# Optimization experiments

Hardware: AMD Instinct MI355X
Metric: run time of the kernel (lower is better)

The kernel has to match this reference:

```python
import jax, jax.numpy as jnp
import numpy as np

# SMPL kinematic tree (24 joints); edge (parent -> child) for each child with parent >= 0
SMPL_PARENTS = np.array([-1, 0, 0, 0, 1, 2, 3, 4, 5, 6, 7, 8, 9, 9, 9, 12, 13, 14, 16, 17, 18, 19, 20, 21])
J = 24            # SMPL_NR_JOINTS
IN_DIM = 3        # input_dim
HID = 24          # hidden_dim
HEADS = 3
OUT = HID // HEADS  # 8 per-head channels; concat -> 24
N, L = 64, 2048
NEG_SLOPE = 0.2   # PyG GATConv default LeakyReLU slope


def _batched_edges(num_frames):
    """Tree edges replicated per (batch, time) frame with node-index offsets."""
    mask = SMPL_PARENTS >= 0
    parent = SMPL_PARENTS[mask]            # source nodes
    child = np.arange(J)[mask]             # destination nodes
    base = np.stack([parent, child])       # (2, 23)
    off = np.arange(num_frames) * J        # (num_frames,)
    edges = base[:, None, :] + off[None, :, None]   # (2, num_frames, 23)
    return edges.reshape(2, -1).astype(np.int32)


def setup_inputs() -> dict:
    key = jax.random.key(0)
    ks = jax.random.split(key, 7)
    s_pre = 1.0 / np.sqrt(IN_DIM)
    s_gat = 1.0 / np.sqrt(HID)
    return {
        "src": jax.random.normal(ks[0], (N, L, J * IN_DIM), dtype=jnp.float32),
        "W_pre": jax.random.normal(ks[1], (IN_DIM, HID), dtype=jnp.float32) * s_pre,
        "b_pre": jax.random.normal(ks[2], (HID,), dtype=jnp.float32) * s_pre,
        "W_gat": jax.random.normal(ks[3], (HID, HEADS * OUT), dtype=jnp.float32) * s_gat,
        "att_src": jax.random.normal(ks[4], (HEADS, OUT), dtype=jnp.float32) * s_gat,
        "att_dst": jax.random.normal(ks[5], (HEADS, OUT), dtype=jnp.float32) * s_gat,
        "b_gat": jax.random.normal(ks[6], (HEADS * OUT,), dtype=jnp.float32) * s_gat,
    }


def reference(src, W_pre, b_pre, W_gat, att_src, att_dst, b_gat):
    n, l, d = src.shape
    num_frames = n * l
    nn = num_frames * J                       # total nodes
    x = src.reshape(nn, IN_DIM)
    x = jax.nn.relu(x @ W_pre + b_pre)        # (nn, 24)

    # GATConv (shared lin for src/dst since single in_channels)
    h = (x @ W_gat).reshape(nn, HEADS, OUT)   # (nn, H, O)
    a_src = jnp.einsum('nho,ho->nh', h, att_src)  # (nn, H)
    a_dst = jnp.einsum('nho,ho->nh', h, att_dst)

    tree = jnp.asarray(_batched_edges(num_frames))          # (2, 23*frames)
    loops = jnp.arange(nn, dtype=jnp.int32)                  # PyG default add_self_loops=True
    src_i = jnp.concatenate([tree[0], loops])
    dst_i = jnp.concatenate([tree[1], loops])

    e = jax.nn.leaky_relu(a_src[src_i] + a_dst[dst_i], NEG_SLOPE)   # (E, H)
    m = jax.ops.segment_max(e, dst_i, num_segments=nn)
    ex = jnp.exp(e - m[dst_i])
    denom = jax.ops.segment_sum(ex, dst_i, num_segments=nn)
    alpha = ex / denom[dst_i]                                       # segment softmax over dst

    out = jax.ops.segment_sum(alpha[:, :, None] * h[src_i], dst_i, num_segments=nn)  # (nn, H, O)
    out = out.reshape(nn, HEADS * OUT) + b_gat
    out = jax.nn.relu(out)
    return out.reshape(n, l, J * HID)
```

## Files before the change

kernel.cpp:

```cpp
#include <hip/hip_runtime.h>


#define JNT 24
#define FPB 8
#define TPB (FPB*JNT)
#define NPB (FPB*JNT)
#define NT  16384
#define GRID 1280

__constant__ int c_par[JNT] = {-1,0,0,0,1,2,3,4,5,6,7,8,9,9,9,12,13,14,16,17,18,19,20,21};

__device__ __forceinline__ int hoff(int r) { return r*28 + ((r>>3)<<2); }

#define SH_SIZE 5468

#define BAR() do { asm volatile("s_waitcnt lgkmcnt(0)" ::: "memory"); \
                   __builtin_amdgcn_s_barrier(); } while (0)

__global__ __launch_bounds__(TPB, 4)
void gat_encoder(const float* __restrict__ src,
                 const float* __restrict__ W_pre,
                 const float* __restrict__ b_pre,
                 const float* __restrict__ W_gat,
                 const float* __restrict__ att_src,
                 const float* __restrict__ att_dst,
                 const float* __restrict__ b_gat,
                 float* __restrict__ out)
{
    __shared__ int   s_par[JNT];
    __shared__ __align__(16) float s_h[SH_SIZE];

    const int tid = threadIdx.x;
    if (tid < JNT) s_par[tid] = c_par[tid];

    int tile = blockIdx.x;

    const float* sg = src + (size_t)tile * (NPB*3) + tid*3;
    float p0 = sg[0], p1 = sg[1], p2 = sg[2];

    while (tile < NT) {
        const int nxt = tile + GRID;
        const float* ng = src + (size_t)(nxt < NT ? nxt : tile) * (NPB*3) + tid*3;
        float q0 = ng[0], q1 = ng[1], q2 = ng[2];

        float h[JNT];
        #pragma unroll
        for (int o = 0; o < JNT; ++o) h[o] = 0.f;

        #pragma unroll 2
        for (int k = 0; k < JNT; ++k) {
            const float w0 = W_pre[k], w1 = W_pre[24+k], w2 = W_pre[48+k];
            const float bb = b_pre[k];
            float x = fmaf(p0, w0, fmaf(p1, w1, fmaf(p2, w2, bb)));
            x = fmaxf(x, 0.f);
            #pragma unroll
            for (int o = 0; o < JNT; ++o)
                h[o] = fmaf(x, W_gat[k*JNT + o], h[o]);
        }

        float as[3], ad[3];
        #pragma unroll
        for (int hd = 0; hd < 3; ++hd) {
            float a = 0.f, d = 0.f;
            #pragma unroll
            for (int o = 0; o < 8; ++o) {
                a = fmaf(h[hd*8+o], att_src[hd*8+o], a);
                d = fmaf(h[hd*8+o], att_dst[hd*8+o], d);
            }
            as[hd] = a; ad[hd] = d;
        }

        float* hr = &s_h[hoff(tid)];
        #pragma unroll
        for (int q = 0; q < 6; ++q)
            ((float4*)hr)[q] = make_float4(h[q*4+0], h[q*4+1], h[q*4+2], h[q*4+3]);
        hr[24] = as[0]; hr[25] = as[1]; hr[26] = as[2];
        BAR();

        const int  f    = tid / JNT;
        const int  j    = tid - f*JNT;
        const int  par  = s_par[j];
        const bool hasp = (par >= 0);
        const float* hp = &s_h[hoff(f*JNT + (hasp ? par : j))];

        float ws[3], wpv[3];
        #pragma unroll
        for (int hd = 0; hd < 3; ++hd) {
            float es = as[hd] + ad[hd];      es = es < 0.f ? 0.2f*es : es;
            float ep = hp[24+hd] + ad[hd];   ep = ep < 0.f ? 0.2f*ep : ep;
            float m  = hasp ? fmaxf(es, ep) : es;
            float e1 = __expf(es - m);
            float e2 = hasp ? __expf(ep - m) : 0.f;
            float r  = 1.f / (e1 + e2);
            ws[hd] = e1*r; wpv[hd] = e2*r;
        }

        float r[JNT];
        #pragma unroll
        for (int q = 0; q < 6; ++q) {
            const int hd = q >> 1;
            const float4 p4 = ((const float4*)hp)[q];
            r[q*4+0] = fmaxf(fmaf(wpv[hd], p4.x, fmaf(ws[hd], h[q*4+0], b_gat[q*4+0])), 0.f);
            r[q*4+1] = fmaxf(fmaf(wpv[hd], p4.y, fmaf(ws[hd], h[q*4+1], b_gat[q*4+1])), 0.f);
            r[q*4+2] = fmaxf(fmaf(wpv[hd], p4.z, fmaf(ws[hd], h[q*4+2], b_gat[q*4+2])), 0.f);
            r[q*4+3] = fmaxf(fmaf(wpv[hd], p4.w, fmaf(ws[hd], h[q*4+3], b_gat[q*4+3])), 0.f);
        }

        BAR();
        {
            float* orow = &s_h[tid*28];
            #pragma unroll
            for (int q = 0; q < 6; ++q)
                ((float4*)orow)[q] = make_float4(r[q*4+0], r[q*4+1], r[q*4+2], r[q*4+3]);
        }
        BAR();

        {
            const int n0 = (tid*4) / JNT;
            const int c0 = (tid*4) % JNT;
            const float* rb = &s_h[n0*28 + c0];
            float4 v[6];
            #pragma unroll
            for (int k = 0; k < 6; ++k)
                v[k] = *(const float4*)(rb + k*896);
            float* og = out + (size_t)tile * (NPB*JNT) + tid*4;
            #pragma unroll
            for (int k = 0; k < 6; ++k)
                *(float4*)(og + k*768) = v[k];
        }

        BAR();
        p0 = q0; p1 = q1; p2 = q2;
        tile = nxt;
    }
}

extern "C" void kernel_launch(void* const* d_in, const int* in_sizes, int n_in,
                              void* d_out, int out_size, void* d_ws, size_t ws_size,
                              hipStream_t stream) {
    const float* src     = (const float*)d_in[0];
    const float* W_pre   = (const float*)d_in[1];
    const float* b_pre   = (const float*)d_in[2];
    const float* W_gat   = (const float*)d_in[3];
    const float* att_src = (const float*)d_in[4];
    const float* att_dst = (const float*)d_in[5];
    const float* b_gat   = (const float*)d_in[6];
    float* out = (float*)d_out;

    gat_encoder<<<dim3(GRID), dim3(TPB), 0, stream>>>(
        src, W_pre, b_pre, W_gat, att_src, att_dst, b_gat, out);
}
```

Before: 360.6 us.

## Switch to one-wave blocks of two frames and packed float2 math

The persistent grid-stride kernel with 8-frame, 192-thread blocks and register prefetch is replaced by a non-persistent launch of 65536 single-wave blocks, each handling two frames (48 active lanes of 64). The dense projections and aggregation are rewritten with two-wide float vector types so the compiler can emit packed FMA instructions. The intent is to cut per-instruction ALU cost and let the hardware scheduler hide latency across many small blocks. In exchange, a quarter of the lanes sit idle in compute, the cross-tile prefetch is lost, and launch/block scheduling overhead rises.

```diff
diff --git a/kernel.cpp b/kernel.cpp
--- a/kernel.cpp
+++ b/kernel.cpp
@@ -1,18 +1,19 @@
 #include <hip/hip_runtime.h>
 
 
+typedef float f32x2 __attribute__((ext_vector_type(2)));
+
 #define JNT 24
-#define FPB 8
-#define TPB (FPB*JNT)
-#define NPB (FPB*JNT)
-#define NT  16384
-#define GRID 1280
+#define FPW 2
+#define TPB 64
+#define ACT (FPW*JNT)
+#define OUTD (ACT*JNT)
 
 __constant__ int c_par[JNT] = {-1,0,0,0,1,2,3,4,5,6,7,8,9,9,9,12,13,14,16,17,18,19,20,21};
 
 __device__ __forceinline__ int hoff(int r) { return r*28 + ((r>>3)<<2); }
 
-#define SH_SIZE 5468
+#define SH_SIZE 1364
 
 #define BAR() do { asm volatile("s_waitcnt lgkmcnt(0)" ::: "memory"); \
                    __builtin_amdgcn_s_barrier(); } while (0)
@@ -31,21 +32,20 @@
     __shared__ __align__(16) float s_h[SH_SIZE];
 
     const int tid = threadIdx.x;
+    const int blk = blockIdx.x;
+    const bool act = tid < ACT;
+
     if (tid < JNT) s_par[tid] = c_par[tid];
 
-    int tile = blockIdx.x;
+    f32x2 h2[12];
+    float as[3], ad[3];
 
-    const float* sg = src + (size_t)tile * (NPB*3) + tid*3;
-    float p0 = sg[0], p1 = sg[1], p2 = sg[2];
+    if (act) {
+        const float* sg = src + (size_t)blk * (ACT*3) + tid*3;
+        const float p0 = sg[0], p1 = sg[1], p2 = sg[2];
 
-    while (tile < NT) {
-        const int nxt = tile + GRID;
-        const float* ng = src + (size_t)(nxt < NT ? nxt : tile) * (NPB*3) + tid*3;
-        float q0 = ng[0], q1 = ng[1], q2 = ng[2];
-
-        float h[JNT];
         #pragma unroll
-        for (int o = 0; o < JNT; ++o) h[o] = 0.f;
+        for (int o = 0; o < 12; ++o) h2[o] = (f32x2){0.f, 0.f};
 
         #pragma unroll 2
         for (int k = 0; k < JNT; ++k) {
@@ -53,31 +53,38 @@
             const float bb = b_pre[k];
             float x = fmaf(p0, w0, fmaf(p1, w1, fmaf(p2, w2, bb)));
             x = fmaxf(x, 0.f);
+            const f32x2 xx = (f32x2){x, x};
+            const f32x2* wr = (const f32x2*)(W_gat + k*JNT);
             #pragma unroll
-            for (int o = 0; o < JNT; ++o)
-                h[o] = fmaf(x, W_gat[k*JNT + o], h[o]);
+            for (int o = 0; o < 12; ++o)
+                h2[o] = xx * wr[o] + h2[o];
         }
 
-        float as[3], ad[3];
         #pragma unroll
         for (int hd = 0; hd < 3; ++hd) {
-            float a = 0.f, d = 0.f;
+            f32x2 a2 = (f32x2){0.f, 0.f}, d2 = (f32x2){0.f, 0.f};
+            const f32x2* asr = (const f32x2*)(att_src + hd*8);
+            const f32x2* adr = (const f32x2*)(att_dst + hd*8);
             #pragma unroll
-            for (int o = 0; o < 8; ++o) {
-                a = fmaf(h[hd*8+o], att_src[hd*8+o], a);
-                d = fmaf(h[hd*8+o], att_dst[hd*8+o], d);
+            for (int o = 0; o < 4; ++o) {
+                a2 = h2[hd*4+o] * asr[o] + a2;
+                d2 = h2[hd*4+o] * adr[o] + d2;
             }
-            as[hd] = a; ad[hd] = d;
+            as[hd] = a2.x + a2.y;
+            ad[hd] = d2.x + d2.y;
         }
 
         float* hr = &s_h[hoff(tid)];
         #pragma unroll
         for (int q = 0; q < 6; ++q)
-            ((float4*)hr)[q] = make_float4(h[q*4+0], h[q*4+1], h[q*4+2], h[q*4+3]);
+            ((float4*)hr)[q] = make_float4(h2[2*q].x, h2[2*q].y, h2[2*q+1].x, h2[2*q+1].y);
         hr[24] = as[0]; hr[25] = as[1]; hr[26] = as[2];
-        BAR();
+    }
+    BAR();
 
-        const int  f    = tid / JNT;
+    f32x2 r2[12];
+    if (act) {
+        const int  f    = tid >= JNT;
         const int  j    = tid - f*JNT;
         const int  par  = s_par[j];
         const bool hasp = (par >= 0);
@@ -95,43 +102,49 @@
             ws[hd] = e1*r; wpv[hd] = e2*r;
         }
 
-        float r[JNT];
+        const f32x2* bg = (const f32x2*)b_gat;
         #pragma unroll
         for (int q = 0; q < 6; ++q) {
             const int hd = q >> 1;
             const float4 p4 = ((const float4*)hp)[q];
-            r[q*4+0] = fmaxf(fmaf(wpv[hd], p4.x, fmaf(ws[hd], h[q*4+0], b_gat[q*4+0])), 0.f);
-            r[q*4+1] = fmaxf(fmaf(wpv[hd], p4.y, fmaf(ws[hd], h[q*4+1], b_gat[q*4+1])), 0.f);
-            r[q*4+2] = fmaxf(fmaf(wpv[hd], p4.z, fmaf(ws[hd], h[q*4+2], b_gat[q*4+2])), 0.f);
-            r[q*4+3] = fmaxf(fmaf(wpv[hd], p4.w, fmaf(ws[hd], h[q*4+3], b_gat[q*4+3])), 0.f);
+            const f32x2 wsv = (f32x2){ws[hd],  ws[hd]};
+            const f32x2 wp2 = (f32x2){wpv[hd], wpv[hd]};
+            f32x2 t0 = (f32x2){p4.x, p4.y};
+            f32x2 t1 = (f32x2){p4.z, p4.w};
+            f32x2 a = wp2 * t0 + (wsv * h2[2*q]   + bg[2*q]);
+            f32x2 b = wp2 * t1 + (wsv * h2[2*q+1] + bg[2*q+1]);
+            a.x = fmaxf(a.x, 0.f); a.y = fmaxf(a.y, 0.f);
+            b.x = fmaxf(b.x, 0.f); b.y = fmaxf(b.y, 0.f);
+            r2[2*q] = a; r2[2*q+1] = b;
         }
+    }
+    BAR();
 
-        BAR();
-        {
-            float* orow = &s_h[tid*28];
-            #pragma unroll
-            for (int q = 0; q < 6; ++q)
-                ((float4*)orow)[q] = make_float4(r[q*4+0], r[q*4+1], r[q*4+2], r[q*4+3]);
+    if (act) {
+        float* orow = &s_h[hoff(tid)];
+        #pragma unroll
+        for (int q = 0; q < 6; ++q)
+            ((float4*)orow)[q] = make_float4(r2[2*q].x, r2[2*q].y, r2[2*q+1].x, r2[2*q+1].y);
+    }
+    BAR();
+
+    {
+        float* og = out + (size_t)blk * OUTD;
+        #pragma unroll
+        for (int k = 0; k < 4; ++k) {
+            const int c  = k*64 + tid;
+            const int n0 = (c*4) / JNT;
+            const int o0 = (c*4) - n0*JNT;
+            const float4 v = *(const float4*)&s_h[hoff(n0) + o0];
+            ((float4*)og)[c] = v;
         }
-        BAR();
-
-        {
-            const int n0 = (tid*4) / JNT;
-            const int c0 = (tid*4) % JNT;
-            const float* rb = &s_h[n0*28 + c0];
-            float4 v[6];
-            #pragma unroll
-            for (int k = 0; k < 6; ++k)
-                v[k] = *(const float4*)(rb + k*896);
-            float* og = out + (size_t)tile * (NPB*JNT) + tid*4;
-            #pragma unroll
-            for (int k = 0; k < 6; ++k)
-                *(float4*)(og + k*768) = v[k];
+        if (tid < 32) {
+            const int c  = 256 + tid;
+            const int n0 = (c*4) / JNT;
+            const int o0 = (c*4) - n0*JNT;
+            const float4 v = *(const float4*)&s_h[hoff(n0) + o0];
+            ((float4*)og)[c] = v;
         }
-
-        BAR();
-        p0 = q0; p1 = q1; p2 = q2;
-        tile = nxt;
     }
 }
 
@@ -147,6 +160,8 @@
     const float* b_gat   = (const float*)d_in[6];
     float* out = (float*)d_out;
 
-    gat_encoder<<<dim3(GRID), dim3(TPB), 0, stream>>>(
+    const int frames = 64 * 2048;
+    const int blocks = frames / FPW;
+    gat_encoder<<<dim3(blocks), dim3(TPB), 0, stream>>>(
         src, W_pre, b_pre, W_gat, att_src, att_dst, b_gat, out);
 }
```

Result: no change. 359.8 us (-0.2%).
